# Optimization experiments

Measured on AMD Instinct MI355X. Metric: run time of the kernel, lower is better.

Reference implementation:

```python
import jax, jax.numpy as jnp
import numpy as np

N, E, D, H, T, R, K = 40000, 320000, 128, 4, 3, 5, 3
DK = D // H
SQRT_DK = float(np.sqrt(DK))

def _glorot(key, shape):
    lim = float(np.sqrt(6.0 / (shape[-2] + shape[-1])))
    return jax.random.uniform(key, shape, jnp.float32, -lim, lim)

def setup_inputs():
    ks = jax.random.split(jax.random.key(0), 16)
    return {
        "meta_xs": jax.random.normal(ks[0], (N, D), jnp.float32),
        "node_type": jax.random.randint(ks[1], (N,), 0, T),
        "edge_index": jax.random.randint(ks[2], (2, E), 0, N),
        "edge_type": jax.random.randint(ks[3], (E,), 0, R),
        "edge_time": jax.random.randint(ks[4], (E,), 0, 100),
        "q_w": _glorot(ks[5], (T, D, D)), "q_b": jnp.zeros((T, D), jnp.float32),
        "k_w": _glorot(ks[6], (T, D, D)), "k_b": jnp.zeros((T, D), jnp.float32),
        "v_w": _glorot(ks[7], (T, D, D)), "v_b": jnp.zeros((T, D), jnp.float32),
        "a_w": _glorot(ks[8], (T, D, D)), "a_b": jnp.zeros((T, D), jnp.float32),
        "rel_pri": jnp.ones((R, H), jnp.float32),
        "rel_att": _glorot(ks[9], (R, H, DK, DK)),
        "rel_msg": _glorot(ks[10], (R, H, DK, DK)),
        "WMk": _glorot(ks[11], (K, D, D)),
        "Wak": _glorot(ks[12], (K, D, D)),
        "Wq": _glorot(ks[13], (D, D)), "bq": jnp.zeros((D,), jnp.float32),
        "Wkl": _glorot(ks[14], (D, D)), "bkl": jnp.zeros((D,), jnp.float32),
        "skip": jnp.ones((T,), jnp.float32),
        "ln_g": jnp.ones((T, D), jnp.float32),
        "ln_b": jnp.zeros((T, D), jnp.float32),
    }

def _forward(meta_xs, q_w, q_b, k_w, k_b, v_w, v_b, a_w, a_b, rel_pri, rel_att,
             rel_msg, WMk, Wak, Wq, bq, Wkl, bkl, skip, ln_g, ln_b,
             node_type, edge_index, edge_type):
    src, tgt = edge_index[0], edge_index[1]
    ar = jnp.arange(N)

    def typed(x, W, b):  # per-node-type linear: equivalent to the type-masked loops
        all_t = jnp.einsum('ni,tio->tno', x, W)        # [T, N, D]
        return all_t[node_type, ar] + b[node_type]      # [N, D]

    qn = typed(meta_xs, q_w, q_b).reshape(N, H, DK)
    kn = typed(meta_xs, k_w, k_b).reshape(N, H, DK)
    vn = typed(meta_xs, v_w, v_b).reshape(N, H, DK)
    qe, ke, ve = qn[tgt], kn[src], vn[src]              # [E, H, DK]

    # relation-specific bmm, honoring per-relation dispatch without [E,H,DK,DK] gather
    kp = jnp.zeros_like(ke)
    vp = jnp.zeros_like(ve)
    for r in range(R):
        sel = (edge_type == r)[:, None, None]
        kp = jnp.where(sel, jnp.einsum('ehd,hdm->ehm', ke, rel_att[r]), kp)
        vp = jnp.where(sel, jnp.einsum('ehd,hdm->ehm', ve, rel_msg[r]), vp)

    logits = (qe * kp).sum(-1) * rel_pri[edge_type] / SQRT_DK   # [E, H]
    # segment softmax over incoming edges per target node (torch_geometric softmax)
    mx = jax.ops.segment_max(logits, tgt, num_segments=N)
    ex = jnp.exp(logits - mx[tgt])
    att = ex / (jax.ops.segment_sum(ex, tgt, num_segments=N)[tgt] + 1e-16)

    # power-moment expanded, attention-weighted messages: [K, E, D]
    msgs = jnp.stack([((vp ** (kk + 1)) * att[:, :, None]).reshape(E, D) for kk in range(K)])

    # faithful to original aggregate(): messages indexed by target node id (not edge id)
    agg = jnp.stack([jax.ops.segment_sum(msgs[kk][tgt], tgt, num_segments=N) for kk in range(K)])
    # faithful: only the last moment gets the signed K-th root (loop re-clones each iter)
    root = jnp.sign(agg[K - 1]) * (jnp.abs(agg[K - 1]) + 1e-18) ** (1.0 / K)
    aggm = agg.at[K - 1].set(root)
    aggm = jnp.einsum('knd,kde->kne', aggm, WMk)        # [K, N, D]

    qlin = meta_xs @ Wq + bq
    res = jnp.zeros((N, D), meta_xs.dtype)
    for kk in range(K):
        front = qlin @ Wak[kk]                          # [N, D]
        tail = aggm[kk] @ Wkl + bkl                     # [N, D]
        t = jax.nn.sigmoid((front * tail).sum(-1))      # [N]
        res = res + t[:, None] * aggm[kk]

    # update(): gelu -> per-type linear -> learned skip -> per-type LayerNorm
    h = jax.nn.gelu(res, approximate=False)
    trans = typed(h, a_w, a_b)
    alpha = jax.nn.sigmoid(skip)[node_type][:, None]
    y = trans * alpha + meta_xs * (1.0 - alpha)
    mu = y.mean(-1, keepdims=True)
    var = ((y - mu) ** 2).mean(-1, keepdims=True)
    y = (y - mu) / jnp.sqrt(var + 1e-5) * ln_g[node_type] + ln_b[node_type]
    return y

def reference(meta_xs, node_type, edge_index, edge_type, edge_time,
              q_w, q_b, k_w, k_b, v_w, v_b, a_w, a_b, rel_pri, rel_att, rel_msg,
              WMk, Wak, Wq, bq, Wkl, bkl, skip, ln_g, ln_b):
    return _forward(meta_xs, q_w, q_b, k_w, k_b, v_w, v_b, a_w, a_b, rel_pri,
                    rel_att, rel_msg, WMk, Wak, Wq, bq, Wkl, bkl, skip, ln_g, ln_b,
                    node_type, edge_index, edge_type)
```

## Files before the change

kernel.cpp:

```cpp
#include <hip/hip_runtime.h>

#define N_ 40000
#define E_ 320000
#define D_ 128
#define H_ 4
#define T_ 3
#define R_ 5

typedef unsigned short u16;
typedef float f32x4 __attribute__((ext_vector_type(4)));
typedef short s16x8 __attribute__((ext_vector_type(8)));

__device__ __forceinline__ float bf2f(u16 h){ return __uint_as_float(((unsigned)h)<<16); }
__device__ __forceinline__ u16 f2bf(float f){
  unsigned u = __float_as_uint(f);
  u += 0x7fffu + ((u>>16)&1u);
  return (u16)(u>>16);
}
__device__ __forceinline__ unsigned fmono(float f){
  unsigned u = __float_as_uint(f);
  return (u>>31) ? ~u : (u | 0x80000000u);
}
__device__ __forceinline__ float monof(unsigned u){
  return (u>>31) ? __uint_as_float(u & 0x7fffffffu) : __uint_as_float(~u);
}
__device__ __forceinline__ float ldx(const void* p, long i, int f32){
  return f32 ? ((const float*)p)[i] : bf2f(((const u16*)p)[i]);
}
__device__ __forceinline__ float wredsum(float v){
  #pragma unroll
  for (int m=32;m;m>>=1) v += __shfl_xor(v, m, 64);
  return v;
}
__device__ __forceinline__ void split2(float v0, float v1, unsigned& hp, unsigned& lp){
  unsigned b0 = __float_as_uint(v0), b1 = __float_as_uint(v1);
  unsigned h0 = b0 & 0xFFFF0000u,    h1 = b1 & 0xFFFF0000u;
  float r0 = v0 - __uint_as_float(h0);
  float r1 = v1 - __uint_as_float(h1);
  hp = (h0>>16) | h1;
  lp = (__float_as_uint(r0)>>16) | (__float_as_uint(r1) & 0xFFFF0000u);
}

#define W_QW 0
#define W_KW 49152
#define W_VW 98304
#define W_AW 147456
#define W_QB 196608
#define W_KB 196992
#define W_VB 197376
#define W_AB 197760
#define W_PRI 198144
#define W_RATT 198164
#define W_RMSG 218644
#define W_WMK 239124
#define W_WAK 288276
#define W_WQ 337428
#define W_BQ 353812
#define W_WKL 353940
#define W_BKL 370324
#define W_SKIP 370452
#define W_LNG 370455
#define W_LNB 370839
#define W_TOT 371223

#define WT_Q   0
#define WT_K   98304
#define WT_V   196608
#define WT_A   294912
#define WT_WQ  396328
#define WT_WMK 478248

#define OFF_FLAGS 0ul
#define OFF_WCF   512ul
#define OFF_NT32  1485824ul
#define OFF_EI32  1646080ul
#define OFF_ET32  4206592ul
#define OFF_PERM  5486592ul
#define OFF_PCNT  5648384ul
#define OFF_TVAL  5648896ul
#define OFF_NPERM 5730816ul
#define OFF_LOG   6288896ul
#define OFF_QN    12848896ul
#define OFF_KN    33328896ul
#define OFF_VN    53808896ul
#define OFF_QLIN  74288896ul
#define OFF_QTR   94768896ul

__global__ __launch_bounds__(256) void detect_kernel(
    const u16* __restrict__ xs, const int* __restrict__ nt, int* __restrict__ flags)
{
  __shared__ int sBig, sZero, sNz;
  int tid = threadIdx.x;
  if (tid==0){ sBig=0; sZero=0; sNz=0; }
  __syncthreads();
  int big=0, zc=0;
  for (int i=tid; i<1024; i+=256) {
    u16 v = xs[2*i];
    int e = (v>>7)&0xFF;
    big += (e >= 200);
    zc  += (v == 0);
  }
  int nz=0;
  for (int i=tid; i<1024; i+=256) nz += (nt[2*i+1] != 0);
  atomicAdd(&sBig, big); atomicAdd(&sZero, zc); atomicAdd(&sNz, nz);
  __syncthreads();
  if (tid==0) {
    flags[0] = (sBig > 64) || (sZero > 900);
    flags[1] = (sNz == 0);
  }
}

struct FPtrs { const void* p[20]; };
__global__ __launch_bounds__(256) void convf_kernel(
    const int* __restrict__ flags, FPtrs ptrs, float* __restrict__ wcf)
{
  const int start[21] = {0,49152,98304,147456,196608,196992,197376,197760,198144,
    198164,218644,239124,288276,337428,353812,353940,370324,370452,370455,370839,371223};
  int i = blockIdx.x*256 + threadIdx.x;
  if (i >= W_TOT) return;
  int arr = 0;
  #pragma unroll
  for (int a=1; a<20; ++a) arr += (i >= start[a]);
  int local = i - start[arr];
  wcf[i] = ldx(ptrs.p[arr], local, flags[0]);
}

__global__ __launch_bounds__(256) void idxconv_kernel(
    const int* __restrict__ flags,
    const int* __restrict__ nt, const int* __restrict__ ei, const int* __restrict__ et,
    int* __restrict__ nt32, int* __restrict__ ei32, int* __restrict__ et32)
{
  int i = blockIdx.x*256 + threadIdx.x;
  if (i >= 1000000) return;
  int w = flags[1] ? 2 : 1;
  if (i < 40000)        nt32[i] = nt[(long)i*w];
  else if (i < 680000)  { int j=i-40000;  ei32[j] = ei[(long)j*w]; }
  else                  { int j=i-680000; et32[j] = et[(long)j*w]; }
}

__global__ __launch_bounds__(256) void pinit_kernel(int* __restrict__ perm, int* __restrict__ pc){
  int i = blockIdx.x*256 + threadIdx.x;
  if (i < 40448) perm[i] = -1;
  if (i < 12) pc[i] = 0;
}
__global__ __launch_bounds__(256) void einit_kernel(int* __restrict__ nperm, int* __restrict__ pc2){
  int i = blockIdx.x*256 + threadIdx.x;
  if (i < 40320) nperm[i] = -1;
  if (i < 16) pc2[i] = 0;
}
__global__ __launch_bounds__(256) void cnt_kernel(
    const int* __restrict__ keys, int n, int ntypes, int* __restrict__ gcnt)
{
  __shared__ int lh[8];
  if (threadIdx.x < ntypes) lh[threadIdx.x] = 0;
  __syncthreads();
  int i = blockIdx.x*256 + threadIdx.x;
  if (i < n) atomicAdd(&lh[keys[i]], 1);
  __syncthreads();
  if (threadIdx.x < ntypes && lh[threadIdx.x])
    atomicAdd(&gcnt[threadIdx.x], lh[threadIdx.x]);
}
__global__ void pofs_kernel(int* __restrict__ pc){
  if (threadIdx.x==0 && blockIdx.x==0) {
    pc[8] = 0;
    pc[9] = (pc[0]+127)&~127;
    pc[10] = pc[9] + ((pc[1]+127)&~127);
  }
}
__global__ void eofs_kernel(int* __restrict__ pc2){
  if (threadIdx.x==0 && blockIdx.x==0) {
    pc2[10] = 0;
    #pragma unroll
    for (int r=1;r<R_;++r) pc2[10+r] = pc2[10+r-1] + ((pc2[r-1]+63)&~63);
  }
}
__global__ __launch_bounds__(256) void scat_kernel(
    const int* __restrict__ keys, int n, int ntypes,
    const int* __restrict__ ofs, int* __restrict__ fill, int* __restrict__ perm)
{
  __shared__ int lh[8];
  __shared__ int lbase[8];
  if (threadIdx.x < ntypes) lh[threadIdx.x] = 0;
  __syncthreads();
  int i = blockIdx.x*256 + threadIdx.x;
  int t = 0, rank = 0;
  bool ok = (i < n);
  if (ok) { t = keys[i]; rank = atomicAdd(&lh[t], 1); }
  __syncthreads();
  if (threadIdx.x < ntypes)
    lbase[threadIdx.x] = lh[threadIdx.x] ? atomicAdd(&fill[threadIdx.x], lh[threadIdx.x]) : 0;
  __syncthreads();
  if (ok) perm[ofs[t] + lbase[t] + rank] = i;
}

__global__ __launch_bounds__(256) void init_kernel(
    unsigned* __restrict__ mxkey, float* __restrict__ sumex, int* __restrict__ deg)
{
  int i = blockIdx.x*256 + threadIdx.x;
  mxkey[i] = fmono(-1e30f);
  sumex[i] = 0.f;
  if (i < N_) deg[i] = 0;
}

__global__ __launch_bounds__(256) void prepA_kernel(
    const float* __restrict__ wcf, float* __restrict__ raT)
{
  int i = blockIdx.x*256 + threadIdx.x;
  if (i >= 20480) return;
  int d = i & 31, m = (i>>5) & 31, rh = i >> 10;
  raT[i] = wcf[W_RATT + (rh*32 + d)*32 + m];
}

__global__ __launch_bounds__(128) void prepB_kernel(
    const float* __restrict__ wcf, float* __restrict__ MT, float* __restrict__ ck)
{
  int col = threadIdx.x, i = blockIdx.x, k = blockIdx.y;
  const float* wak = wcf + W_WAK + k*16384 + col*128;
  const float* wkl = wcf + W_WKL + i*128;
  float acc = 0.f, accC = 0.f;
  #pragma unroll 8
  for (int j=0;j<128;++j) {
    float a = wak[j];
    acc  += a * wkl[j];
    if (i==0) accC += a * wcf[W_BKL + j];
  }
  MT[k*16384 + i*128 + col] = acc;
  if (i==0) ck[k*128 + col] = accC;
}

struct TPtrs { const void* p[16]; int soff[16]; int doff[16]; };
__global__ __launch_bounds__(256) void prepT_kernel(
    TPtrs tp, const int* __restrict__ flags, int xmode, u16* __restrict__ dst)
{
  __shared__ float T[128][33];
  int m = blockIdx.y;
  int c0 = blockIdx.x * 32;
  int tid = threadIdx.x;
  int xf = xmode ? 1 : flags[0];
  const void* src = tp.p[m];
  long sb = tp.soff[m];
  {
    int k = tid >> 1, ch = (tid & 1) * 16;
    #pragma unroll
    for (int j=0;j<16;++j)
      T[k][ch+j] = ldx(src, sb + (long)k*128 + c0 + ch + j, xf);
  }
  __syncthreads();
  int col = tid >> 3, k0 = (tid & 7) * 16;
  unsigned hp[8], lp[8];
  #pragma unroll
  for (int j=0;j<8;++j)
    split2(T[k0+2*j][col], T[k0+2*j+1][col], hp[j], lp[j]);
  u16* dh = dst + tp.doff[m] + (long)(c0+col)*128 + k0;
  ((uint4*)dh)[0] = uint4{hp[0],hp[1],hp[2],hp[3]};
  ((uint4*)dh)[1] = uint4{hp[4],hp[5],hp[6],hp[7]};
  u16* dl = dh + 16384;
  ((uint4*)dl)[0] = uint4{lp[0],lp[1],lp[2],lp[3]};
  ((uint4*)dl)[1] = uint4{lp[4],lp[5],lp[6],lp[7]};
}

struct GC4 { const float* x[4]; int woff[4]; int boff[4]; int typed[4]; };
__global__ __launch_bounds__(256) void gemmt2_kernel(
    GC4 cfg, const int* __restrict__ flags, int xmode,
    const u16* __restrict__ Wt, const float* __restrict__ wcf,
    const int* __restrict__ perm, const int* __restrict__ nt,
    int dotmode, const float* __restrict__ qlin, const float* __restrict__ ck,
    int powmode, const float* __restrict__ sattp, int wmode,
    float* __restrict__ out, long yostride)
{
  int tid = threadIdx.x;
  int y = blockIdx.y;
  int row0 = blockIdx.x*128;
  int lane = tid & 63;
  int wv   = tid >> 6;
  int lrow = lane & 15;
  int lk   = (lane >> 4) << 3;
  int rbase = wv*32;

  int head = perm ? perm[row0] : (row0 < N_ ? row0 : -1);
  if (head < 0) return;
  int tblk = (cfg.typed[y] && perm && nt) ? nt[head] : 0;
  const u16* Wg = Wt + cfg.woff[y] + tblk*32768;
  const void* X = (const void*)cfg.x[y];
  int xf = xmode ? 1 : flags[0];
  int wlo_on = wmode ? 1 : flags[0];

  int rl0 = row0 + rbase + lrow;
  int rl1 = rl0 + 16;
  int sr0 = perm ? perm[rl0] : (rl0 < N_ ? rl0 : -1);
  int sr1 = perm ? perm[rl1] : (rl1 < N_ ? rl1 : -1);
  long s0 = (sr0 < 0) ? 0 : (long)sr0;
  long s1 = (sr1 < 0) ? 0 : (long)sr1;

  f32x4 acc[2][8];
  #pragma unroll
  for (int m=0;m<2;++m)
    #pragma unroll
    for (int n=0;n<8;++n) acc[m][n] = f32x4{0.f,0.f,0.f,0.f};

  #pragma unroll
  for (int kc=0;kc<4;++kc) {
    s16x8 ah0, ah1, al0, al1;
    if (xf) {
      const float* x0 = (const float*)X + s0*128 + kc*32 + lk;
      const float* x1 = (const float*)X + s1*128 + kc*32 + lk;
      float4 a0 = ((const float4*)x0)[0], a1 = ((const float4*)x0)[1];
      float4 b0 = ((const float4*)x1)[0], b1 = ((const float4*)x1)[1];
      float t0[8] = {a0.x,a0.y,a0.z,a0.w,a1.x,a1.y,a1.z,a1.w};
      float t1[8] = {b0.x,b0.y,b0.z,b0.w,b1.x,b1.y,b1.z,b1.w};
      if (powmode) {
        float sc0 = sattp[s0*4 + kc];
        float sc1 = sattp[s1*4 + kc];
        #pragma unroll
        for (int j=0;j<8;++j) {
          float v0 = t0[j], v1 = t1[j];
          if (y==0)      { t0[j] = v0*sc0;    t1[j] = v1*sc1; }
          else if (y==1) { t0[j] = v0*v0*sc0; t1[j] = v1*v1*sc1; }
          else {
            float a3 = v0*v0*v0*sc0, b3 = v1*v1*v1*sc1;
            t0[j] = (a3==0.f) ? 0.f : copysignf(cbrtf(fabsf(a3)+1e-18f), a3);
            t1[j] = (b3==0.f) ? 0.f : copysignf(cbrtf(fabsf(b3)+1e-18f), b3);
          }
        }
      }
      unsigned h0[4], l0[4], h1[4], l1[4];
      #pragma unroll
      for (int j=0;j<4;++j) {
        split2(t0[2*j], t0[2*j+1], h0[j], l0[j]);
        split2(t1[2*j], t1[2*j+1], h1[j], l1[j]);
      }
      uint4 H0{h0[0],h0[1],h0[2],h0[3]}, L0{l0[0],l0[1],l0[2],l0[3]};
      uint4 H1{h1[0],h1[1],h1[2],h1[3]}, L1{l1[0],l1[1],l1[2],l1[3]};
      ah0 = *reinterpret_cast<s16x8*>(&H0); al0 = *reinterpret_cast<s16x8*>(&L0);
      ah1 = *reinterpret_cast<s16x8*>(&H1); al1 = *reinterpret_cast<s16x8*>(&L1);
    } else {
      ah0 = *reinterpret_cast<const s16x8*>((const u16*)X + s0*128 + kc*32 + lk);
      ah1 = *reinterpret_cast<const s16x8*>((const u16*)X + s1*128 + kc*32 + lk);
    }
    #pragma unroll
    for (int n=0;n<8;++n) {
      const u16* wp = Wg + (n*16+lrow)*128 + kc*32 + lk;
      s16x8 bh = *reinterpret_cast<const s16x8*>(wp);
      acc[0][n] = __builtin_amdgcn_mfma_f32_16x16x32_bf16(ah0, bh, acc[0][n], 0,0,0);
      acc[1][n] = __builtin_amdgcn_mfma_f32_16x16x32_bf16(ah1, bh, acc[1][n], 0,0,0);
      if (xf) {
        acc[0][n] = __builtin_amdgcn_mfma_f32_16x16x32_bf16(al0, bh, acc[0][n], 0,0,0);
        acc[1][n] = __builtin_amdgcn_mfma_f32_16x16x32_bf16(al1, bh, acc[1][n], 0,0,0);
      }
      if (wlo_on) {
        s16x8 bl = *reinterpret_cast<const s16x8*>(wp + 16384);
        acc[0][n] = __builtin_amdgcn_mfma_f32_16x16x32_bf16(ah0, bl, acc[0][n], 0,0,0);
        acc[1][n] = __builtin_amdgcn_mfma_f32_16x16x32_bf16(ah1, bl, acc[1][n], 0,0,0);
      }
    }
  }

  int rq = (lane >> 4) << 2;
  if (!dotmode) {
    float b[8];
    if (cfg.boff[y] >= 0) {
      const float* bp = wcf + cfg.boff[y] + tblk*128;
      #pragma unroll
      for (int n=0;n<8;++n) b[n] = bp[n*16 + lrow];
    } else {
      #pragma unroll
      for (int n=0;n<8;++n) b[n] = 0.f;
    }
    #pragma unroll
    for (int m=0;m<2;++m) {
      #pragma unroll
      for (int r=0;r<4;++r) {
        int rr = row0 + rbase + m*16 + rq + r;
        int rowg = perm ? perm[rr] : (rr < N_ ? rr : -1);
        if (rowg < 0) continue;
        float* op = out + (long)y*yostride + (long)rowg*128 + lrow;
        #pragma unroll
        for (int n=0;n<8;++n) op[n*16] = acc[m][n][r] + b[n];
      }
    }
  } else {
    float ckv[8];
    #pragma unroll
    for (int n=0;n<8;++n) ckv[n] = ck[y*128 + n*16 + lrow];
    #pragma unroll
    for (int m=0;m<2;++m) {
      #pragma unroll
      for (int r=0;r<4;++r) {
        int rr = row0 + rbase + m*16 + rq + r;
        int rowg = perm ? perm[rr] : (rr < N_ ? rr : -1);
        float d = 0.f;
        if (rowg >= 0) {
          const float* qp = qlin + (long)rowg*128 + lrow;
          #pragma unroll
          for (int n=0;n<8;++n) d += (acc[m][n][r] + ckv[n]) * qp[n*16];
        }
        #pragma unroll
        for (int msk=1; msk<16; msk<<=1) d += __shfl_xor(d, msk, 64);
        if (lrow==0 && rowg>=0) out[(long)rowg*4 + y] = 1.f/(1.f+expf(-d));
      }
    }
  }
}

__global__ __launch_bounds__(256) void gemmbd_kernel(
    const float* __restrict__ X,
    const float* __restrict__ Wtab, int wsel,
    const int* __restrict__ perm, const int* __restrict__ gsrc, const int* __restrict__ et,
    float* __restrict__ out)
{
  __shared__ float As[64*152];
  __shared__ float Ws[4096];
  __shared__ int ridx[64];
  __shared__ int rsel_s;
  int tid = threadIdx.x;
  int row0 = blockIdx.x*64;
  if (tid < 64) {
    int rr = row0 + tid;
    int pe = perm ? perm[rr] : (rr < N_ ? rr : -1);
    ridx[tid] = pe;
    if (tid == 0) rsel_s = (wsel && pe >= 0) ? et[pe] : 0;
  }
  __syncthreads();
  if (ridx[0] < 0) return;
  const float* Wg = Wtab + (long)(wsel ? rsel_s : 0)*4096;
  #pragma unroll
  for (int j=0;j<4;++j)
    *reinterpret_cast<float4*>(&Ws[j*1024 + tid*4]) =
      *reinterpret_cast<const float4*>(Wg + j*1024 + tid*4);
  {
    int sar = tid >> 2, sh = tid & 3;
    int pe_s = ridx[sar];
    int arow = (pe_s < 0) ? -1 : (gsrc ? gsrc[pe_s] : pe_s);
    float* dst = &As[sar*152 + sh*36];
    if (arow < 0) {
      #pragma unroll
      for (int j=0;j<8;++j) *reinterpret_cast<float4*>(dst + j*4) = float4{0.f,0.f,0.f,0.f};
    } else {
      const float4* s4 = reinterpret_cast<const float4*>(X + (long)arow*128 + sh*32);
      #pragma unroll
      for (int j=0;j<8;++j) *reinterpret_cast<float4*>(dst + j*4) = s4[j];
    }
  }
  __syncthreads();
  int rg_ = tid >> 5, cg = tid & 31;
  int h = cg >> 3, c4 = (cg & 7)*4;
  float acc[8][4];
  #pragma unroll
  for (int r=0;r<8;++r){ acc[r][0]=0.f; acc[r][1]=0.f; acc[r][2]=0.f; acc[r][3]=0.f; }
  #pragma unroll
  for (int mq=0;mq<8;++mq) {
    float wv[4][4];
    #pragma unroll
    for (int i=0;i<4;++i) {
      float4 wt = *reinterpret_cast<const float4*>(&Ws[h*1024 + (mq*4+i)*32 + c4]);
      wv[i][0]=wt.x; wv[i][1]=wt.y; wv[i][2]=wt.z; wv[i][3]=wt.w;
    }
    #pragma unroll
    for (int r=0;r<8;++r) {
      float4 a4 = *reinterpret_cast<const float4*>(&As[(rg_*8+r)*152 + h*36 + mq*4]);
      float av[4] = {a4.x,a4.y,a4.z,a4.w};
      #pragma unroll
      for (int i=0;i<4;++i) {
        acc[r][0]+=av[i]*wv[i][0]; acc[r][1]+=av[i]*wv[i][1];
        acc[r][2]+=av[i]*wv[i][2]; acc[r][3]+=av[i]*wv[i][3];
      }
    }
  }
  #pragma unroll
  for (int r=0;r<8;++r) {
    int pe = ridx[rg_*8+r];
    if (pe < 0) continue;
    float4 o = {acc[r][0],acc[r][1],acc[r][2],acc[r][3]};
    *reinterpret_cast<float4*>(out + (long)pe*128 + h*32 + c4) = o;
  }
}

__global__ __launch_bounds__(256) void epass_kernel(
    const float* __restrict__ kn, const float* __restrict__ qtr, const float* __restrict__ wcf,
    const int* __restrict__ ei, const int* __restrict__ et, int rsel,
    float* __restrict__ logits, unsigned* __restrict__ mxkey, int* __restrict__ deg)
{
  int gid = blockIdx.x*256 + threadIdx.x;
  int e = gid >> 2, h = gid & 3;
  if (et[e] != rsel) return;
  int s = ei[e], t = ei[E_+e];
  const float4* ka = reinterpret_cast<const float4*>(kn + (long)s*128 + h*32);
  const float4* qa = reinterpret_cast<const float4*>(qtr + (long)t*128 + h*32);
  float acc = 0.f;
  #pragma unroll
  for (int i=0;i<8;++i) {
    float4 a = ka[i], b = qa[i];
    acc += a.x*b.x + a.y*b.y + a.z*b.z + a.w*b.w;
  }
  float lg = acc * wcf[W_PRI + rsel*H_+h] * 0.17677669529663687f;
  logits[gid] = lg;
  atomicMax(mxkey + t*H_+h, fmono(lg));
  if (h==0) atomicAdd(deg + t, 1);
}

__global__ __launch_bounds__(256) void eexp_kernel(
    const int* __restrict__ ei, float* __restrict__ logits,
    const unsigned* __restrict__ mxkey, float* __restrict__ sumex)
{
  int gid = blockIdx.x*256 + threadIdx.x;
  int e = gid >> 2, h = gid & 3;
  int t = ei[E_+e];
  float d = fminf(logits[gid] - monof(mxkey[t*H_+h]), 0.f);
  float ex = expf(d);
  if (e < N_) logits[gid] = ex;
  atomicAdd(sumex + t*H_+h, ex);
}

__global__ __launch_bounds__(256) void satt_kernel(
    const int* __restrict__ ei, const float* __restrict__ ex, const float* __restrict__ sumex,
    const int* __restrict__ deg, float* __restrict__ satt)
{
  int i = blockIdx.x*256 + threadIdx.x;
  int n = i >> 2, h = i & 3;
  int t = ei[E_+n];
  satt[i] = (float)deg[n] * ex[i] / (sumex[t*H_+h] + 1e-16f);
}

__global__ __launch_bounds__(256) void gatemix_kernel(
    const float* __restrict__ tval,
    const float* __restrict__ ag0, const float* __restrict__ ag1, const float* __restrict__ ag2,
    float* __restrict__ hout)
{
  long gid = (long)blockIdx.x*256 + threadIdx.x;
  int n = (int)(gid >> 7);
  float res = tval[n*4+0]*ag0[gid] + tval[n*4+1]*ag1[gid] + tval[n*4+2]*ag2[gid];
  hout[gid] = 0.5f*res*(1.f+erff(res*0.70710678118654752f));
}

__global__ __launch_bounds__(256) void lnf_kernel(
    const float* __restrict__ trans, const void* __restrict__ x, const int* __restrict__ flags,
    const int* __restrict__ nt, const float* __restrict__ wcf, void* __restrict__ outv)
{
  int wave = threadIdx.x >> 6, lane = threadIdx.x & 63;
  int n = blockIdx.x*4 + wave;
  int j = lane*2;
  int xf = flags[0];
  int t = nt[n];
  float alpha = 1.f/(1.f+expf(-wcf[W_SKIP+t]));
  long base = (long)n*128 + j;
  float y0 = alpha*trans[base]   + (1.f-alpha)*ldx(x, base,   xf);
  float y1 = alpha*trans[base+1] + (1.f-alpha)*ldx(x, base+1, xf);
  float mu = wredsum(y0+y1) * (1.f/128.f);
  float d0 = y0-mu, d1 = y1-mu;
  float var = wredsum(d0*d0+d1*d1) * (1.f/128.f);
  float inv = rsqrtf(var + 1e-5f);
  float o0 = d0*inv*wcf[W_LNG + t*128+j]   + wcf[W_LNB + t*128+j];
  float o1 = d1*inv*wcf[W_LNG + t*128+j+1] + wcf[W_LNB + t*128+j+1];
  if (xf) {
    ((float*)outv)[base]   = o0;
    ((float*)outv)[base+1] = o1;
  } else {
    unsigned o = (unsigned)f2bf(o0) | ((unsigned)f2bf(o1)<<16);
    *reinterpret_cast<unsigned*>(((u16*)outv)+base) = o;
  }
}

extern "C" void kernel_launch(void* const* d_in, const int* in_sizes, int n_in,
                              void* d_out, int out_size, void* d_ws, size_t ws_size,
                              hipStream_t stream) {
  char* w = (char*)d_ws;
  int*      flags = (int*)     (w + OFF_FLAGS);
  float*    wcf   = (float*)   (w + OFF_WCF);
  u16*      wtb   = (u16*)     (w + OFF_WCF);
  int*      nt32  = (int*)     (w + OFF_NT32);
  int*      ei32  = (int*)     (w + OFF_EI32);
  int*      et32  = (int*)     (w + OFF_ET32);
  int*      perm  = (int*)     (w + OFF_PERM);
  int*      pcnt  = (int*)     (w + OFF_PCNT);
  int*      pc2   = (int*)     (w + OFF_PCNT + 128);
  float*    raT   = (float*)   (w + OFF_TVAL);
  float*    satt  = (float*)   (w + OFF_TVAL);
  float*    tval  = (float*)   (w + OFF_TVAL);
  int*      nperm = (int*)     (w + OFF_NPERM);
  float*    logits= (float*)   (w + OFF_LOG);
  unsigned* mxkey = (unsigned*)(w + OFF_LOG + 5120000);
  float*    sumex = (float*)   (w + OFF_LOG + 5760000);
  int*      deg   = (int*)     (w + OFF_LOG + 6400000);
  float*    MT    = (float*)   (w + OFF_LOG);
  float*    ckb   = (float*)   (w + OFF_LOG + 786432);
  u16*      mtt   = (u16*)     (w + OFF_LOG + 1048576);
  float*    qn    = (float*)   (w + OFF_QN);
  float*    ag0   = (float*)   (w + OFF_QN);
  float*    trans = (float*)   (w + OFF_QN);
  float*    kn    = (float*)   (w + OFF_KN);
  float*    ag1   = (float*)   (w + OFF_KN);
  float*    vn    = (float*)   (w + OFF_VN);
  float*    ag2   = (float*)   (w + OFF_VN);
  float*    qlin  = (float*)   (w + OFF_QLIN);
  float*    hbuf  = (float*)   (w + OFF_QLIN);
  float*    qtrb  = (float*)   (w + OFF_QTR);
  float*    vp    = (float*)   (w + OFF_QTR);

  detect_kernel<<<1,256,0,stream>>>((const u16*)d_in[0], (const int*)d_in[1], flags);
  FPtrs fp;
  fp.p[0]=d_in[5];  fp.p[1]=d_in[7];  fp.p[2]=d_in[9];  fp.p[3]=d_in[11];
  fp.p[4]=d_in[6];  fp.p[5]=d_in[8];  fp.p[6]=d_in[10]; fp.p[7]=d_in[12];
  fp.p[8]=d_in[13]; fp.p[9]=d_in[14]; fp.p[10]=d_in[15];fp.p[11]=d_in[16];
  fp.p[12]=d_in[17];fp.p[13]=d_in[18];fp.p[14]=d_in[19];fp.p[15]=d_in[20];
  fp.p[16]=d_in[21];fp.p[17]=d_in[22];fp.p[18]=d_in[23];fp.p[19]=d_in[24];
  convf_kernel<<<1451,256,0,stream>>>(flags, fp, wcf);
  idxconv_kernel<<<3907,256,0,stream>>>(flags, (const int*)d_in[1],
                                        (const int*)d_in[2], (const int*)d_in[3],
                                        nt32, ei32, et32);
  pinit_kernel<<<159,256,0,stream>>>(perm, pcnt);
  cnt_kernel  <<<157,256,0,stream>>>(nt32, N_, T_, pcnt);
  pofs_kernel <<<1,64,0,stream>>>(pcnt);
  scat_kernel <<<157,256,0,stream>>>(nt32, N_, T_, pcnt+8, pcnt+4, perm);
  einit_kernel<<<158,256,0,stream>>>(nperm, pc2);
  cnt_kernel  <<<157,256,0,stream>>>(et32, N_, R_, pc2);
  eofs_kernel <<<1,64,0,stream>>>(pc2);
  scat_kernel <<<157,256,0,stream>>>(et32, N_, R_, pc2+10, pc2+5, nperm);
  prepA_kernel<<<80,256,0,stream>>>(wcf, raT);

  TPtrs tps;
  for (int t=0;t<3;++t) {
    tps.p[t]    = d_in[5];  tps.soff[t]    = t*16384; tps.doff[t]    = WT_Q   + t*32768;
    tps.p[3+t]  = d_in[7];  tps.soff[3+t]  = t*16384; tps.doff[3+t]  = WT_K   + t*32768;
    tps.p[6+t]  = d_in[9];  tps.soff[6+t]  = t*16384; tps.doff[6+t]  = WT_V   + t*32768;
    tps.p[9+t]  = d_in[11]; tps.soff[9+t]  = t*16384; tps.doff[9+t]  = WT_A   + t*32768;
    tps.p[13+t] = d_in[16]; tps.soff[13+t] = t*16384; tps.doff[13+t] = WT_WMK + t*32768;
  }
  tps.p[12] = d_in[18]; tps.soff[12] = 0; tps.doff[12] = WT_WQ;
  prepT_kernel<<<dim3(4,16),256,0,stream>>>(tps, flags, 0, wtb);

  GC4 cq;
  cq.x[0]=(const float*)d_in[0]; cq.x[1]=cq.x[0]; cq.x[2]=cq.x[0]; cq.x[3]=cq.x[0];
  cq.woff[0]=WT_Q; cq.woff[1]=WT_K; cq.woff[2]=WT_V; cq.woff[3]=WT_WQ;
  cq.boff[0]=W_QB; cq.boff[1]=W_KB; cq.boff[2]=W_VB; cq.boff[3]=W_BQ;
  cq.typed[0]=1; cq.typed[1]=1; cq.typed[2]=1; cq.typed[3]=0;
  gemmt2_kernel<<<dim3(316,4),256,0,stream>>>(cq, flags, 0, wtb, wcf, perm, nt32,
      0, nullptr, nullptr, 0, nullptr, 0, qn, 5120000);

  init_kernel<<<625,256,0,stream>>>(mxkey, sumex, deg);

  for (int r=0; r<R_; ++r) {
    gemmbd_kernel<<<625,256,0,stream>>>(qn, raT + r*4096, 0, nullptr, nullptr, nullptr, qtrb);
    epass_kernel<<<5000,256,0,stream>>>(kn, qtrb, wcf, ei32, et32, r, logits, mxkey, deg);
  }
  eexp_kernel<<<5000,256,0,stream>>>(ei32, logits, mxkey, sumex);

  gemmbd_kernel<<<630,256,0,stream>>>(vn, wcf+W_RMSG, 1, nperm, ei32, et32, vp);

  satt_kernel<<<625,256,0,stream>>>(ei32, logits, sumex, deg, satt);

  prepB_kernel<<<dim3(128,3),128,0,stream>>>(wcf, MT, ckb);
  TPtrs tpm;
  for (int i=0;i<16;++i){ tpm.p[i]=MT; tpm.soff[i]=0; tpm.doff[i]=0; }
  for (int k=0;k<3;++k){ tpm.soff[k]=k*16384; tpm.doff[k]=k*32768; }
  prepT_kernel<<<dim3(4,3),256,0,stream>>>(tpm, flags, 1, mtt);

  GC4 cp;
  cp.x[0]=vp; cp.x[1]=vp; cp.x[2]=vp; cp.x[3]=vp;
  cp.woff[0]=WT_WMK; cp.woff[1]=WT_WMK+32768; cp.woff[2]=WT_WMK+65536; cp.woff[3]=0;
  cp.boff[0]=-1; cp.boff[1]=-1; cp.boff[2]=-1; cp.boff[3]=-1;
  cp.typed[0]=0; cp.typed[1]=0; cp.typed[2]=0; cp.typed[3]=0;
  gemmt2_kernel<<<dim3(313,3),256,0,stream>>>(cp, flags, 1, wtb, wcf, nullptr, nullptr,
      0, nullptr, nullptr, 1, satt, 0, ag0, 5120000);

  GC4 cd;
  cd.x[0]=ag0; cd.x[1]=ag1; cd.x[2]=ag2; cd.x[3]=ag2;
  cd.woff[0]=0; cd.woff[1]=32768; cd.woff[2]=65536; cd.woff[3]=0;
  cd.boff[0]=-1; cd.boff[1]=-1; cd.boff[2]=-1; cd.boff[3]=-1;
  cd.typed[0]=0; cd.typed[1]=0; cd.typed[2]=0; cd.typed[3]=0;
  gemmt2_kernel<<<dim3(313,3),256,0,stream>>>(cd, flags, 1, mtt, wcf, nullptr, nullptr,
      1, qlin, ckb, 0, nullptr, 1, tval, 0);

  gatemix_kernel<<<20000,256,0,stream>>>(tval, ag0, ag1, ag2, hbuf);

  GC4 ct;
  ct.x[0]=hbuf; ct.x[1]=hbuf; ct.x[2]=hbuf; ct.x[3]=hbuf;
  ct.woff[0]=WT_A; ct.woff[1]=0; ct.woff[2]=0; ct.woff[3]=0;
  ct.boff[0]=W_AB; ct.boff[1]=-1; ct.boff[2]=-1; ct.boff[3]=-1;
  ct.typed[0]=1; ct.typed[1]=0; ct.typed[2]=0; ct.typed[3]=0;
  gemmt2_kernel<<<dim3(316,1),256,0,stream>>>(ct, flags, 1, wtb, wcf, perm, nt32,
      0, nullptr, nullptr, 0, nullptr, 0, trans, 0);

  lnf_kernel<<<10000,256,0,stream>>>(trans, d_in[0], flags, nt32, wcf, d_out);

  (void)in_sizes; (void)n_in; (void)out_size; (void)ws_size;
}
```

Baseline: 657.6 us.

## Stage weight tiles in swizzled LDS with register prefetch in gemmt2 kernel

The typed GEMM kernel now loads each 32-wide K-chunk of the bf16 weight (hi and lo parts) cooperatively into XOR-swizzled shared memory once per block, instead of every wave reading the weights from global memory. Activations and weights for the next K-chunk are prefetched into registers while the current chunk is computed. The row permutation indices are also cached in shared memory for the gather and the epilogue. This adds two barriers per chunk and more register and LDS use, which may reduce occupancy, in exchange for less redundant global and L2 weight traffic.

```diff
diff --git a/kernel.cpp b/kernel.cpp
--- a/kernel.cpp
+++ b/kernel.cpp
@@ -268,29 +268,42 @@
     int powmode, const float* __restrict__ sattp, int wmode,
     float* __restrict__ out, long yostride)
 {
+  __shared__ u16 Wh[4096], Wl[4096];
+  __shared__ int ridx[128];
+  __shared__ int tblk_s;
   int tid = threadIdx.x;
   int y = blockIdx.y;
   int row0 = blockIdx.x*128;
+  if (tid < 128) {
+    int rr = row0 + tid;
+    int rg = perm ? perm[rr] : (rr < N_ ? rr : -1);
+    ridx[tid] = rg;
+    if (tid==0) tblk_s = (perm && nt && rg>=0) ? nt[rg] : 0;
+  }
+  __syncthreads();
+  if (ridx[0] < 0) return;
+  int tblk = cfg.typed[y] ? tblk_s : 0;
+  const u16* Wg = Wt + cfg.woff[y] + tblk*32768;
+  const void* X = (const void*)cfg.x[y];
+  int xf = xmode ? 1 : flags[0];
+  int wlo_on = wmode ? 1 : flags[0];
+
   int lane = tid & 63;
   int wv   = tid >> 6;
   int lrow = lane & 15;
   int lk   = (lane >> 4) << 3;
   int rbase = wv*32;
 
-  int head = perm ? perm[row0] : (row0 < N_ ? row0 : -1);
-  if (head < 0) return;
-  int tblk = (cfg.typed[y] && perm && nt) ? nt[head] : 0;
-  const u16* Wg = Wt + cfg.woff[y] + tblk*32768;
-  const void* X = (const void*)cfg.x[y];
-  int xf = xmode ? 1 : flags[0];
-  int wlo_on = wmode ? 1 : flags[0];
-
-  int rl0 = row0 + rbase + lrow;
-  int rl1 = rl0 + 16;
-  int sr0 = perm ? perm[rl0] : (rl0 < N_ ? rl0 : -1);
-  int sr1 = perm ? perm[rl1] : (rl1 < N_ ? rl1 : -1);
-  long s0 = (sr0 < 0) ? 0 : (long)sr0;
-  long s1 = (sr1 < 0) ? 0 : (long)sr1;
+  int sr0i = ridx[rbase + lrow];
+  int sr1i = ridx[rbase + lrow + 16];
+  long s0 = (sr0i < 0) ? 0 : (long)sr0i;
+  long s1 = (sr1i < 0) ? 0 : (long)sr1i;
+
+  int sr = tid >> 1;
+  int sh = (tid & 1) * 16;
+  int sp  = (sr >> 1) & 3;
+  int sc0 = (sh >> 3) ^ sp;
+  int sc1 = ((sh >> 3) + 1) ^ sp;
 
   f32x4 acc[2][8];
   #pragma unroll
@@ -298,26 +311,39 @@
     #pragma unroll
     for (int n=0;n<8;++n) acc[m][n] = f32x4{0.f,0.f,0.f,0.f};
 
-  #pragma unroll
+  float4 fa0, fa1, fb0, fb1;
+  uint4  ua = {0,0,0,0}, ub = {0,0,0,0};
+  float  scp0 = 0.f, scp1 = 0.f;
+  uint4  pw0, pw1, pw2 = {0,0,0,0}, pw3 = {0,0,0,0};
+
+  if (xf) {
+    const float4* x0 = reinterpret_cast<const float4*>((const float*)X + s0*128 + lk);
+    const float4* x1 = reinterpret_cast<const float4*>((const float*)X + s1*128 + lk);
+    fa0=x0[0]; fa1=x0[1]; fb0=x1[0]; fb1=x1[1];
+    if (powmode) { scp0 = sattp[s0*4]; scp1 = sattp[s1*4]; }
+  } else {
+    ua = *reinterpret_cast<const uint4*>((const u16*)X + s0*128 + lk);
+    ub = *reinterpret_cast<const uint4*>((const u16*)X + s1*128 + lk);
+  }
+  {
+    const u16* gh = Wg + sr*128 + sh;
+    pw0 = ((const uint4*)gh)[0]; pw1 = ((const uint4*)gh)[1];
+    if (wlo_on) { pw2 = ((const uint4*)(gh+16384))[0]; pw3 = ((const uint4*)(gh+16384))[1]; }
+  }
+
   for (int kc=0;kc<4;++kc) {
     s16x8 ah0, ah1, al0, al1;
     if (xf) {
-      const float* x0 = (const float*)X + s0*128 + kc*32 + lk;
-      const float* x1 = (const float*)X + s1*128 + kc*32 + lk;
-      float4 a0 = ((const float4*)x0)[0], a1 = ((const float4*)x0)[1];
-      float4 b0 = ((const float4*)x1)[0], b1 = ((const float4*)x1)[1];
-      float t0[8] = {a0.x,a0.y,a0.z,a0.w,a1.x,a1.y,a1.z,a1.w};
-      float t1[8] = {b0.x,b0.y,b0.z,b0.w,b1.x,b1.y,b1.z,b1.w};
+      float t0[8] = {fa0.x,fa0.y,fa0.z,fa0.w, fa1.x,fa1.y,fa1.z,fa1.w};
+      float t1[8] = {fb0.x,fb0.y,fb0.z,fb0.w, fb1.x,fb1.y,fb1.z,fb1.w};
       if (powmode) {
-        float sc0 = sattp[s0*4 + kc];
-        float sc1 = sattp[s1*4 + kc];
         #pragma unroll
         for (int j=0;j<8;++j) {
           float v0 = t0[j], v1 = t1[j];
-          if (y==0)      { t0[j] = v0*sc0;    t1[j] = v1*sc1; }
-          else if (y==1) { t0[j] = v0*v0*sc0; t1[j] = v1*v1*sc1; }
+          if (y==0)      { t0[j] = v0*scp0;    t1[j] = v1*scp1; }
+          else if (y==1) { t0[j] = v0*v0*scp0; t1[j] = v1*v1*scp1; }
           else {
-            float a3 = v0*v0*v0*sc0, b3 = v1*v1*v1*sc1;
+            float a3 = v0*v0*v0*scp0, b3 = v1*v1*v1*scp1;
             t0[j] = (a3==0.f) ? 0.f : copysignf(cbrtf(fabsf(a3)+1e-18f), a3);
             t1[j] = (b3==0.f) ? 0.f : copysignf(cbrtf(fabsf(b3)+1e-18f), b3);
           }
@@ -334,13 +360,39 @@
       ah0 = *reinterpret_cast<s16x8*>(&H0); al0 = *reinterpret_cast<s16x8*>(&L0);
       ah1 = *reinterpret_cast<s16x8*>(&H1); al1 = *reinterpret_cast<s16x8*>(&L1);
     } else {
-      ah0 = *reinterpret_cast<const s16x8*>((const u16*)X + s0*128 + kc*32 + lk);
-      ah1 = *reinterpret_cast<const s16x8*>((const u16*)X + s1*128 + kc*32 + lk);
-    }
+      ah0 = *reinterpret_cast<s16x8*>(&ua);
+      ah1 = *reinterpret_cast<s16x8*>(&ub);
+    }
+    uint4 WH0 = pw0, WH1 = pw1, WL0 = pw2, WL1 = pw3;
+
+    __syncthreads();
+    ((uint4*)Wh)[sr*4 + sc0] = WH0;
+    ((uint4*)Wh)[sr*4 + sc1] = WH1;
+    if (wlo_on) {
+      ((uint4*)Wl)[sr*4 + sc0] = WL0;
+      ((uint4*)Wl)[sr*4 + sc1] = WL1;
+    }
+    if (kc < 3) {
+      int kn_ = kc + 1;
+      if (xf) {
+        const float4* x0 = reinterpret_cast<const float4*>((const float*)X + s0*128 + kn_*32 + lk);
+        const float4* x1 = reinterpret_cast<const float4*>((const float*)X + s1*128 + kn_*32 + lk);
+        fa0=x0[0]; fa1=x0[1]; fb0=x1[0]; fb1=x1[1];
+        if (powmode) { scp0 = sattp[s0*4 + kn_]; scp1 = sattp[s1*4 + kn_]; }
+      } else {
+        ua = *reinterpret_cast<const uint4*>((const u16*)X + s0*128 + kn_*32 + lk);
+        ub = *reinterpret_cast<const uint4*>((const u16*)X + s1*128 + kn_*32 + lk);
+      }
+      const u16* gh = Wg + sr*128 + kn_*32 + sh;
+      pw0 = ((const uint4*)gh)[0]; pw1 = ((const uint4*)gh)[1];
+      if (wlo_on) { pw2 = ((const uint4*)(gh+16384))[0]; pw3 = ((const uint4*)(gh+16384))[1]; }
+    }
+    __syncthreads();
     #pragma unroll
     for (int n=0;n<8;++n) {
-      const u16* wp = Wg + (n*16+lrow)*128 + kc*32 + lk;
-      s16x8 bh = *reinterpret_cast<const s16x8*>(wp);
+      int col = n*16 + lrow;
+      int ib = col*32 + (lk ^ (((col>>1)&3)<<3));
+      s16x8 bh = *(const s16x8*)(Wh + ib);
       acc[0][n] = __builtin_amdgcn_mfma_f32_16x16x32_bf16(ah0, bh, acc[0][n], 0,0,0);
       acc[1][n] = __builtin_amdgcn_mfma_f32_16x16x32_bf16(ah1, bh, acc[1][n], 0,0,0);
       if (xf) {
@@ -348,7 +400,7 @@
         acc[1][n] = __builtin_amdgcn_mfma_f32_16x16x32_bf16(al1, bh, acc[1][n], 0,0,0);
       }
       if (wlo_on) {
-        s16x8 bl = *reinterpret_cast<const s16x8*>(wp + 16384);
+        s16x8 bl = *(const s16x8*)(Wl + ib);
         acc[0][n] = __builtin_amdgcn_mfma_f32_16x16x32_bf16(ah0, bl, acc[0][n], 0,0,0);
         acc[1][n] = __builtin_amdgcn_mfma_f32_16x16x32_bf16(ah1, bl, acc[1][n], 0,0,0);
       }
@@ -370,8 +422,8 @@
     for (int m=0;m<2;++m) {
       #pragma unroll
       for (int r=0;r<4;++r) {
-        int rr = row0 + rbase + m*16 + rq + r;
-        int rowg = perm ? perm[rr] : (rr < N_ ? rr : -1);
+        int rowl = rbase + m*16 + rq + r;
+        int rowg = ridx[rowl];
         if (rowg < 0) continue;
         float* op = out + (long)y*yostride + (long)rowg*128 + lrow;
         #pragma unroll
@@ -386,8 +438,8 @@
     for (int m=0;m<2;++m) {
       #pragma unroll
       for (int r=0;r<4;++r) {
-        int rr = row0 + rbase + m*16 + rq + r;
-        int rowg = perm ? perm[rr] : (rr < N_ ? rr : -1);
+        int rowl = rbase + m*16 + rq + r;
+        int rowg = ridx[rowl];
         float d = 0.f;
         if (rowg >= 0) {
           const float* qp = qlin + (long)rowg*128 + lrow;
```

Result: faster. 544.1 us (-17.3%).
